# Optimization experiments

Hardware: AMD Instinct MI355X
Metric: run time of the kernel (lower is better)

## Reference

```python
import jax, jax.numpy as jnp
import numpy as np

B, C_IN, H, W = 8, 32, 64, 64
C = 64  # num_channels


def setup_inputs() -> dict:
    key = jax.random.key(0)
    ks = jax.random.split(key, 9)
    s_in = 1.0 / np.sqrt(C_IN)
    s_c = 1.0 / np.sqrt(C)
    return {
        "x": jax.random.normal(ks[0], (B, C_IN, H, W), dtype=jnp.float32),
        "wq": jax.random.uniform(ks[1], (C, C_IN), jnp.float32, -s_in, s_in),
        "bq": jax.random.uniform(ks[2], (C,), jnp.float32, -s_in, s_in),
        "wk": jax.random.uniform(ks[3], (C, C_IN), jnp.float32, -s_in, s_in),
        "bk": jax.random.uniform(ks[4], (C,), jnp.float32, -s_in, s_in),
        "wv": jax.random.uniform(ks[5], (C, C_IN), jnp.float32, -s_in, s_in),
        "bv": jax.random.uniform(ks[6], (C,), jnp.float32, -s_in, s_in),
        "wo": jax.random.uniform(ks[7], (C_IN, C), jnp.float32, -s_c, s_c),
        "bo": jax.random.uniform(ks[8], (C_IN,), jnp.float32, -s_c, s_c),
    }


def reference(x, wq, bq, wk, bk, wv, bv, wo, bo):
    b, c_in, h, w = x.shape
    n = h * w
    # 1x1 convs == per-pixel linear projections; produce (B, N, C) directly
    q = (jnp.einsum('bchw,oc->bhwo', x, wq) + bq).reshape(b, n, -1)
    k = (jnp.einsum('bchw,oc->bhwo', x, wk) + bk).reshape(b, n, -1)
    v = (jnp.einsum('bchw,oc->bhwo', x, wv) + bv).reshape(b, n, -1)
    # unscaled attention over spatial positions (no 1/sqrt(d) in original)
    scores = jnp.einsum('bnc,bmc->bnm', q, k)  # (B, N, N)
    attn = jax.nn.softmax(scores, axis=-1)
    out = jnp.einsum('bnm,bmc->bnc', attn, v)  # (B, N, C)
    out = out.reshape(b, h, w, -1)
    out = jnp.einsum('bhwc,oc->bohw', out, wo) + bo[None, :, None, None]
    return out + x
```

## Files before the change

kernel.cpp:

```cpp
#include <hip/hip_runtime.h>
#include <hip/hip_bf16.h>

#define CIN    32
#define NPIX   4096
#define DIM    64
#define LOG2E  1.4426950408889634f

#if __has_builtin(__builtin_amdgcn_exp2f)
#define EXP2(x) __builtin_amdgcn_exp2f(x)
#else
#define EXP2(x) exp2f(x)
#endif

typedef float  f32x4 __attribute__((ext_vector_type(4)));
typedef short  s16x8 __attribute__((ext_vector_type(8)));
typedef short  s16x4 __attribute__((ext_vector_type(4)));

__device__ __forceinline__ f32x4 mfma16(s16x4 a, s16x4 b, f32x4 c) {
#if __has_builtin(__builtin_amdgcn_mfma_f32_16x16x16bf16_1k)
    return __builtin_amdgcn_mfma_f32_16x16x16bf16_1k(a, b, c, 0, 0, 0);
#elif __has_builtin(__builtin_amdgcn_mfma_f32_16x16x16_bf16)
    return __builtin_amdgcn_mfma_f32_16x16x16_bf16(a, b, c, 0, 0, 0);
#else
    f32x4 d;
    asm("v_mfma_f32_16x16x16_bf16 %0, %1, %2, %3" : "=v"(d) : "v"(a), "v"(b), "v"(c));
    return d;
#endif
}


__global__ __launch_bounds__(256) void qkv_proj(
    const float* __restrict__ x,
    const float* __restrict__ wq, const float* __restrict__ bq,
    const float* __restrict__ wk, const float* __restrict__ bk,
    const float* __restrict__ wv, const float* __restrict__ bv,
    __hip_bfloat16* __restrict__ qb, __hip_bfloat16* __restrict__ kb,
    __hip_bfloat16* __restrict__ vb)
{
    __shared__ float Xs[CIN][64];
    __shared__ float wT[3][CIN][DIM];

    const int tid = threadIdx.x;
    const int b   = blockIdx.y;
    const int bx  = blockIdx.x;
    const int n0  = bx * 64;

    for (int i = tid; i < 3 * CIN * DIM; i += 256) {
        int m = i >> 11, r = i & 2047, c = r >> 6, o = r & 63;
        const float* wsrc = (m == 0) ? wq : (m == 1) ? wk : wv;
        float wv0 = wsrc[o * CIN + c];
        wT[m][c][o] = (m == 0) ? wv0 * LOG2E : wv0;
    }
    for (int i = tid * 4; i < CIN * 64; i += 1024) {
        int c = i >> 6, p = i & 63;
        *(f32x4*)&Xs[c][p] = *(const f32x4*)&x[((size_t)b * CIN + c) * NPIX + n0 + p];
    }
    __syncthreads();

    const int w    = tid >> 6;
    const int lane = tid & 63;
    const int l16  = lane >> 2;
    const int quad = lane & 3;

    const int T  = bx * 4 + w;
    const int px = T * 16 + l16;

    float aq[2][8], ak[2][8];
    #pragma unroll
    for (int kb2 = 0; kb2 < 2; kb2++) {
        f32x4 bq0 = *(const f32x4*)&bq[kb2 * 32 + quad * 8];
        f32x4 bq1 = *(const f32x4*)&bq[kb2 * 32 + quad * 8 + 4];
        f32x4 bk0 = *(const f32x4*)&bk[kb2 * 32 + quad * 8];
        f32x4 bk1 = *(const f32x4*)&bk[kb2 * 32 + quad * 8 + 4];
        #pragma unroll
        for (int j = 0; j < 4; j++) {
            aq[kb2][j] = bq0[j] * LOG2E; aq[kb2][j + 4] = bq1[j] * LOG2E;
            ak[kb2][j] = bk0[j];         ak[kb2][j + 4] = bk1[j];
        }
    }
    #pragma unroll 8
    for (int c = 0; c < CIN; c++) {
        const float xc = Xs[c][w * 16 + l16];
        #pragma unroll
        for (int kb2 = 0; kb2 < 2; kb2++) {
            f32x4 q0 = *(const f32x4*)&wT[0][c][kb2 * 32 + quad * 8];
            f32x4 q1 = *(const f32x4*)&wT[0][c][kb2 * 32 + quad * 8 + 4];
            f32x4 k0 = *(const f32x4*)&wT[1][c][kb2 * 32 + quad * 8];
            f32x4 k1 = *(const f32x4*)&wT[1][c][kb2 * 32 + quad * 8 + 4];
            #pragma unroll
            for (int j = 0; j < 4; j++) {
                aq[kb2][j]     += xc * q0[j];
                aq[kb2][j + 4] += xc * q1[j];
                ak[kb2][j]     += xc * k0[j];
                ak[kb2][j + 4] += xc * k1[j];
            }
        }
    }
    #pragma unroll
    for (int kb2 = 0; kb2 < 2; kb2++) {
        union { s16x8 v; __hip_bfloat16 h[8]; } pq, pk;
        #pragma unroll
        for (int j = 0; j < 8; j++) {
            pq.h[j] = __float2bfloat16(aq[kb2][j]);
            pk.h[j] = __float2bfloat16(ak[kb2][j]);
        }
        *(s16x8*)(qb + ((size_t)b * NPIX + px) * DIM + kb2 * 32 + quad * 8) = pq.v;
        const size_t koff =
            ((((size_t)(b * 256 + T) * 2 + kb2) * 16 + l16) * 4 + quad) * 8;
        *(s16x8*)(kb + koff) = pk.v;
    }

    const int ch = w * 16 + l16;
    float av[2][8];
    {
        const float bvc = bv[ch];
        #pragma unroll
        for (int kh = 0; kh < 2; kh++)
            #pragma unroll
            for (int j = 0; j < 8; j++) av[kh][j] = bvc;
    }
    #pragma unroll 8
    for (int c = 0; c < CIN; c++) {
        const float wvc = wT[2][c][ch];
        f32x4 x0 = *(const f32x4*)&Xs[c][quad * 8];
        f32x4 x1 = *(const f32x4*)&Xs[c][quad * 8 + 4];
        f32x4 x2 = *(const f32x4*)&Xs[c][32 + quad * 8];
        f32x4 x3 = *(const f32x4*)&Xs[c][32 + quad * 8 + 4];
        #pragma unroll
        for (int j = 0; j < 4; j++) {
            av[0][j]     += x0[j] * wvc;
            av[0][j + 4] += x1[j] * wvc;
            av[1][j]     += x2[j] * wvc;
            av[1][j + 4] += x3[j] * wvc;
        }
    }
    #pragma unroll
    for (int kh = 0; kh < 2; kh++) {
        #pragma unroll
        for (int h = 0; h < 2; h++) {
            union { unsigned long long u; __hip_bfloat16 hh[4]; } pv;
            #pragma unroll
            for (int j = 0; j < 4; j++) pv.hh[j] = __float2bfloat16(av[kh][h * 4 + j]);
            const int lanep = ((quad & 1) * 2 + h) * 16 + l16;
            const size_t chunk =
                (((size_t)(b * 128 + bx * 2 + kh) * 4 + w) * 64 + lanep) * 2 + (quad >> 1);
            *(unsigned long long*)(vb + chunk * 4) = pv.u;
        }
    }
}

__global__ __launch_bounds__(256, 4) void attn_fused(
    const __hip_bfloat16* __restrict__ qb,
    const __hip_bfloat16* __restrict__ kbf,
    const __hip_bfloat16* __restrict__ vbf,
    const float* __restrict__ wo, const float* __restrict__ bo,
    const float* __restrict__ x, float* __restrict__ y)
{
    __shared__ __align__(16) float RED[4][2][64][18];
    __shared__ float LRED[4][2][16];

    const int tid  = threadIdx.x;
    const int kq   = tid >> 6;
    const int lane = tid & 63;
    const int quad = lane >> 4, l16 = lane & 15;
    const int b    = blockIdx.x;
    const int row0 = blockIdx.y * 32;

    s16x8 qf[2][2];
    #pragma unroll
    for (int mt = 0; mt < 2; mt++)
        #pragma unroll
        for (int kb2 = 0; kb2 < 2; kb2++)
            qf[mt][kb2] = *(const s16x8*)(qb
                + ((size_t)b * NPIX + row0 + mt * 16 + l16) * DIM + kb2 * 32 + quad * 8);

    const f32x4 zero4 = {0.f, 0.f, 0.f, 0.f};
    f32x4 o[2][4];
    #pragma unroll
    for (int mt = 0; mt < 2; mt++)
        #pragma unroll
        for (int ct = 0; ct < 4; ct++) o[mt][ct] = zero4;
    f32x4 ol[2] = {zero4, zero4};

    s16x4 ones;
    #pragma unroll
    for (int j = 0; j < 4; j++) ones[j] = (short)0x3F80;

    const char* kp = (const char*)kbf + (size_t)b * 524288 + kq * 131072
                     + (l16 * 4 + quad) * 16;
    const char* vp = (const char*)vbf + (size_t)b * 524288 + kq * 131072
                     + lane * 16;

    s16x8 ck[4], cv[4];
    #pragma unroll
    for (int i = 0; i < 4; i++) {
        ck[i] = *(const s16x8*)(kp + i * 1024);
        cv[i] = *(const s16x8*)(vp + i * 1024);
    }

    for (int t = 0; t < 32; ++t) {
        kp += 4096; vp += 4096;
        f32x4 st[2][2];
        #pragma unroll
        for (int nt = 0; nt < 2; nt++)
            #pragma unroll
            for (int mt = 0; mt < 2; mt++) {
                st[nt][mt] = __builtin_amdgcn_mfma_f32_16x16x32_bf16(
                    ck[nt * 2 + 0], qf[mt][0], zero4, 0, 0, 0);
                st[nt][mt] = __builtin_amdgcn_mfma_f32_16x16x32_bf16(
                    ck[nt * 2 + 1], qf[mt][1], st[nt][mt], 0, 0, 0);
            }
        #pragma unroll
        for (int i = 0; i < 4; i++) ck[i] = *(const s16x8*)(kp + i * 1024);

        s16x4 pb[2][2];
        #pragma unroll
        for (int nt = 0; nt < 2; nt++)
            #pragma unroll
            for (int mt = 0; mt < 2; mt++) {
                f32x4 p = st[nt][mt];
                #pragma unroll
                for (int r = 0; r < 4; r++) p[r] = EXP2(p[r]);
                union { unsigned int d[2]; s16x4 v; } pk;
                pk.d[0] = (__float_as_uint(p[1]) & 0xffff0000u)
                        | (__float_as_uint(p[0]) >> 16);
                pk.d[1] = (__float_as_uint(p[3]) & 0xffff0000u)
                        | (__float_as_uint(p[2]) >> 16);
                pb[nt][mt] = pk.v;
            }

        #pragma unroll
        for (int ct = 0; ct < 4; ct++) {
            s16x4 vlo = __builtin_shufflevector(cv[ct], cv[ct], 0, 1, 2, 3);
            s16x4 vhi = __builtin_shufflevector(cv[ct], cv[ct], 4, 5, 6, 7);
            #pragma unroll
            for (int mt = 0; mt < 2; mt++) {
                o[mt][ct] = mfma16(vlo, pb[0][mt], o[mt][ct]);
                o[mt][ct] = mfma16(vhi, pb[1][mt], o[mt][ct]);
            }
        }
        #pragma unroll
        for (int mt = 0; mt < 2; mt++) {
            ol[mt] = mfma16(ones, pb[0][mt], ol[mt]);
            ol[mt] = mfma16(ones, pb[1][mt], ol[mt]);
        }
        #pragma unroll
        for (int i = 0; i < 4; i++) cv[i] = *(const s16x8*)(vp + i * 1024);
    }

    #pragma unroll
    for (int mt = 0; mt < 2; mt++) {
        #pragma unroll
        for (int ct = 0; ct < 4; ct++)
            #pragma unroll
            for (int r = 0; r < 4; r++)
                RED[kq][mt][ct * 16 + quad * 4 + r][l16] = o[mt][ct][r];
        if (quad == 0) LRED[kq][mt][l16] = ol[mt][0];
    }
    __syncthreads();

    const int emt = kq >> 1, ent = kq & 1;
    float osum[4][4];
    float lsum = 0.f;
    #pragma unroll
    for (int ct = 0; ct < 4; ct++)
        #pragma unroll
        for (int r = 0; r < 4; r++) osum[ct][r] = 0.f;
    #pragma unroll
    for (int k2 = 0; k2 < 4; k2++) {
        lsum += LRED[k2][emt][l16];
        #pragma unroll
        for (int ct = 0; ct < 4; ct++)
            #pragma unroll
            for (int r = 0; r < 4; r++)
                osum[ct][r] += RED[k2][emt][ct * 16 + quad * 4 + r][l16];
    }

    const float inv = 1.0f / lsum;
    s16x4 pvo[4];
    #pragma unroll
    for (int ct = 0; ct < 4; ct++) {
        union { s16x4 v; __hip_bfloat16 h[4]; } pk;
        #pragma unroll
        for (int r = 0; r < 4; r++)
            pk.h[r] = __float2bfloat16(osum[ct][r] * inv);
        pvo[ct] = pk.v;
    }

    s16x4 aw[4];
    #pragma unroll
    for (int ct = 0; ct < 4; ct++) {
        f32x4 w4 = *(const f32x4*)(wo + (size_t)(ent * 16 + l16) * DIM
                                   + ct * 16 + quad * 4);
        union { s16x4 v; __hip_bfloat16 h[4]; } wf;
        #pragma unroll
        for (int j = 0; j < 4; j++) wf.h[j] = __float2bfloat16(w4[j]);
        aw[ct] = wf.v;
    }

    f32x4 d2 = zero4;
    #pragma unroll
    for (int ct = 0; ct < 4; ct++)
        d2 = mfma16(aw[ct], pvo[ct], d2);

    #pragma unroll
    for (int r = 0; r < 4; r++) {
        const int out = ent * 16 + quad * 4 + r;
        const int row = row0 + emt * 16 + l16;
        const size_t xi = ((size_t)b * CIN + out) * NPIX + row;
        y[xi] = d2[r] + bo[out] + x[xi];
    }
}

extern "C" void kernel_launch(void* const* d_in, const int* in_sizes, int n_in,
                              void* d_out, int out_size, void* d_ws, size_t ws_size,
                              hipStream_t stream)
{
    const float* x  = (const float*)d_in[0];
    const float* wq = (const float*)d_in[1];
    const float* bq = (const float*)d_in[2];
    const float* wk = (const float*)d_in[3];
    const float* bk = (const float*)d_in[4];
    const float* wv = (const float*)d_in[5];
    const float* bv = (const float*)d_in[6];
    const float* wo = (const float*)d_in[7];
    const float* bo = (const float*)d_in[8];
    float* y = (float*)d_out;

    char* ws = (char*)d_ws;
    __hip_bfloat16* qb = (__hip_bfloat16*)(ws);
    __hip_bfloat16* kb = (__hip_bfloat16*)(ws + (4u << 20));
    __hip_bfloat16* vb = (__hip_bfloat16*)(ws + (8u << 20));

    qkv_proj<<<dim3(64, 8), dim3(256), 0, stream>>>(x, wq, bq, wk, bk, wv, bv, qb, kb, vb);
    attn_fused<<<dim3(8, 128), dim3(256), 0, stream>>>(qb, kb, vb, wo, bo, x, y);
}
```

Before: 137.7 us.

## Switch attention kernel to 32x32x16 MFMA tiles with re-laid-out K/V

Replaces the 16x16 MFMA tiling of the fused attention kernel with 32x32x16 bf16 MFMAs. The K and V bf16 buffers written by the projection kernel get new layouts to match. The row sum is now accumulated with scalar adds and a cross-lane shuffle instead of an MFMA against a ones vector. The cross-wave reduction is restructured so wave 0 sums the partials and alone runs the output projection and residual add. The aim is fewer MFMA issues and less shared-memory traffic per tile, at the cost of more accumulator registers and occupancy lowered from 4 to 3 blocks per CU.

```diff
diff --git a/kernel.cpp b/kernel.cpp
--- a/kernel.cpp
+++ b/kernel.cpp
@@ -12,20 +12,14 @@
 #define EXP2(x) exp2f(x)
 #endif
 
-typedef float  f32x4 __attribute__((ext_vector_type(4)));
-typedef short  s16x8 __attribute__((ext_vector_type(8)));
-typedef short  s16x4 __attribute__((ext_vector_type(4)));
-
-__device__ __forceinline__ f32x4 mfma16(s16x4 a, s16x4 b, f32x4 c) {
-#if __has_builtin(__builtin_amdgcn_mfma_f32_16x16x16bf16_1k)
-    return __builtin_amdgcn_mfma_f32_16x16x16bf16_1k(a, b, c, 0, 0, 0);
-#elif __has_builtin(__builtin_amdgcn_mfma_f32_16x16x16_bf16)
-    return __builtin_amdgcn_mfma_f32_16x16x16_bf16(a, b, c, 0, 0, 0);
-#else
-    f32x4 d;
-    asm("v_mfma_f32_16x16x16_bf16 %0, %1, %2, %3" : "=v"(d) : "v"(a), "v"(b), "v"(c));
-    return d;
-#endif
+typedef float  f32x4  __attribute__((ext_vector_type(4)));
+typedef float  f32x16 __attribute__((ext_vector_type(16)));
+typedef short  s16x8  __attribute__((ext_vector_type(8)));
+
+#define ZERO16 {0.f,0.f,0.f,0.f,0.f,0.f,0.f,0.f,0.f,0.f,0.f,0.f,0.f,0.f,0.f,0.f}
+
+__device__ __forceinline__ f32x16 mfma32(s16x8 a, s16x8 b, f32x16 c) {
+    return __builtin_amdgcn_mfma_f32_32x32x16_bf16(a, b, c, 0, 0, 0);
 }
 
 
@@ -96,18 +90,24 @@
             }
         }
     }
-    #pragma unroll
-    for (int kb2 = 0; kb2 < 2; kb2++) {
-        union { s16x8 v; __hip_bfloat16 h[8]; } pq, pk;
-        #pragma unroll
-        for (int j = 0; j < 8; j++) {
-            pq.h[j] = __float2bfloat16(aq[kb2][j]);
-            pk.h[j] = __float2bfloat16(ak[kb2][j]);
-        }
-        *(s16x8*)(qb + ((size_t)b * NPIX + px) * DIM + kb2 * 32 + quad * 8) = pq.v;
-        const size_t koff =
-            ((((size_t)(b * 256 + T) * 2 + kb2) * 16 + l16) * 4 + quad) * 8;
-        *(s16x8*)(kb + koff) = pk.v;
+    {
+        const int s   = px >> 5;
+        const int key = px & 31;
+        #pragma unroll
+        for (int kb2 = 0; kb2 < 2; kb2++) {
+            union { s16x8 v; __hip_bfloat16 h[8]; } pq, pk;
+            #pragma unroll
+            for (int j = 0; j < 8; j++) {
+                pq.h[j] = __float2bfloat16(aq[kb2][j]);
+                pk.h[j] = __float2bfloat16(ak[kb2][j]);
+            }
+            *(s16x8*)(qb + ((size_t)b * NPIX + px) * DIM + kb2 * 32 + quad * 8) = pq.v;
+            const int kt = kb2 * 2 + (quad >> 1);
+            const int h  = quad & 1;
+            const size_t koff = (size_t)b * 262144
+                + ((size_t)(s * 4 + kt) * 64 + h * 32 + key) * 8;
+            *(s16x8*)(kb + koff) = pk.v;
+        }
     }
 
     const int ch = w * 16 + l16;
@@ -136,179 +136,161 @@
     }
     #pragma unroll
     for (int kh = 0; kh < 2; kh++) {
+        const int s = bx * 2 + kh;
         #pragma unroll
         for (int h = 0; h < 2; h++) {
             union { unsigned long long u; __hip_bfloat16 hh[4]; } pv;
             #pragma unroll
             for (int j = 0; j < 4; j++) pv.hh[j] = __float2bfloat16(av[kh][h * 4 + j]);
-            const int lanep = ((quad & 1) * 2 + h) * 16 + l16;
-            const size_t chunk =
-                (((size_t)(b * 128 + bx * 2 + kh) * 4 + w) * 64 + lanep) * 2 + (quad >> 1);
-            *(unsigned long long*)(vb + chunk * 4) = pv.u;
+            const size_t voff = (size_t)b * 262144
+                + ((((size_t)(s * 2 + (ch >> 5)) * 2 + h) * 32 + (ch & 31)) * 2
+                   + (quad >> 1)) * 8
+                + 4 * (quad & 1);
+            *(unsigned long long*)(vb + voff) = pv.u;
         }
     }
 }
 
-__global__ __launch_bounds__(256, 4) void attn_fused(
+__global__ __launch_bounds__(256, 3) void attn_fused(
     const __hip_bfloat16* __restrict__ qb,
     const __hip_bfloat16* __restrict__ kbf,
     const __hip_bfloat16* __restrict__ vbf,
     const float* __restrict__ wo, const float* __restrict__ bo,
     const float* __restrict__ x, float* __restrict__ y)
 {
-    __shared__ __align__(16) float RED[4][2][64][18];
-    __shared__ float LRED[4][2][16];
+    __shared__ __align__(16) float RED[3][64][33];
+    __shared__ float LRED[3][32];
 
     const int tid  = threadIdx.x;
     const int kq   = tid >> 6;
     const int lane = tid & 63;
-    const int quad = lane >> 4, l16 = lane & 15;
+    const int q    = lane & 31;
+    const int hl   = lane >> 5;
     const int b    = blockIdx.x;
     const int row0 = blockIdx.y * 32;
 
-    s16x8 qf[2][2];
+    s16x8 qf[4];
     #pragma unroll
-    for (int mt = 0; mt < 2; mt++)
-        #pragma unroll
-        for (int kb2 = 0; kb2 < 2; kb2++)
-            qf[mt][kb2] = *(const s16x8*)(qb
-                + ((size_t)b * NPIX + row0 + mt * 16 + l16) * DIM + kb2 * 32 + quad * 8);
-
-    const f32x4 zero4 = {0.f, 0.f, 0.f, 0.f};
-    f32x4 o[2][4];
+    for (int kt = 0; kt < 4; kt++)
+        qf[kt] = *(const s16x8*)(qb + ((size_t)b * NPIX + row0 + q) * DIM
+                                 + kt * 16 + hl * 8);
+
+    f32x16 o0 = ZERO16, o1 = ZERO16;
+    float lsacc = 0.f;
+
+    const char* kp = (const char*)kbf + (size_t)b * 524288 + kq * 131072
+                     + (size_t)lane * 16;
+    const char* vp = (const char*)vbf + (size_t)b * 524288 + kq * 131072
+                     + (size_t)lane * 32;
+
+    s16x8 kA[4], kB[4], cv[4];
     #pragma unroll
-    for (int mt = 0; mt < 2; mt++)
-        #pragma unroll
-        for (int ct = 0; ct < 4; ct++) o[mt][ct] = zero4;
-    f32x4 ol[2] = {zero4, zero4};
-
-    s16x4 ones;
-    #pragma unroll
-    for (int j = 0; j < 4; j++) ones[j] = (short)0x3F80;
-
-    const char* kp = (const char*)kbf + (size_t)b * 524288 + kq * 131072
-                     + (l16 * 4 + quad) * 16;
-    const char* vp = (const char*)vbf + (size_t)b * 524288 + kq * 131072
-                     + lane * 16;
-
-    s16x8 ck[4], cv[4];
-    #pragma unroll
-    for (int i = 0; i < 4; i++) {
-        ck[i] = *(const s16x8*)(kp + i * 1024);
-        cv[i] = *(const s16x8*)(vp + i * 1024);
-    }
-
-    for (int t = 0; t < 32; ++t) {
-        kp += 4096; vp += 4096;
-        f32x4 st[2][2];
-        #pragma unroll
-        for (int nt = 0; nt < 2; nt++)
-            #pragma unroll
-            for (int mt = 0; mt < 2; mt++) {
-                st[nt][mt] = __builtin_amdgcn_mfma_f32_16x16x32_bf16(
-                    ck[nt * 2 + 0], qf[mt][0], zero4, 0, 0, 0);
-                st[nt][mt] = __builtin_amdgcn_mfma_f32_16x16x32_bf16(
-                    ck[nt * 2 + 1], qf[mt][1], st[nt][mt], 0, 0, 0);
-            }
-        #pragma unroll
-        for (int i = 0; i < 4; i++) ck[i] = *(const s16x8*)(kp + i * 1024);
-
-        s16x4 pb[2][2];
-        #pragma unroll
-        for (int nt = 0; nt < 2; nt++)
-            #pragma unroll
-            for (int mt = 0; mt < 2; mt++) {
-                f32x4 p = st[nt][mt];
-                #pragma unroll
-                for (int r = 0; r < 4; r++) p[r] = EXP2(p[r]);
-                union { unsigned int d[2]; s16x4 v; } pk;
-                pk.d[0] = (__float_as_uint(p[1]) & 0xffff0000u)
-                        | (__float_as_uint(p[0]) >> 16);
-                pk.d[1] = (__float_as_uint(p[3]) & 0xffff0000u)
-                        | (__float_as_uint(p[2]) >> 16);
-                pb[nt][mt] = pk.v;
-            }
-
-        #pragma unroll
-        for (int ct = 0; ct < 4; ct++) {
-            s16x4 vlo = __builtin_shufflevector(cv[ct], cv[ct], 0, 1, 2, 3);
-            s16x4 vhi = __builtin_shufflevector(cv[ct], cv[ct], 4, 5, 6, 7);
-            #pragma unroll
-            for (int mt = 0; mt < 2; mt++) {
-                o[mt][ct] = mfma16(vlo, pb[0][mt], o[mt][ct]);
-                o[mt][ct] = mfma16(vhi, pb[1][mt], o[mt][ct]);
-            }
-        }
-        #pragma unroll
-        for (int mt = 0; mt < 2; mt++) {
-            ol[mt] = mfma16(ones, pb[0][mt], ol[mt]);
-            ol[mt] = mfma16(ones, pb[1][mt], ol[mt]);
-        }
-        #pragma unroll
-        for (int i = 0; i < 4; i++) cv[i] = *(const s16x8*)(vp + i * 1024);
-    }
-
-    #pragma unroll
-    for (int mt = 0; mt < 2; mt++) {
-        #pragma unroll
-        for (int ct = 0; ct < 4; ct++)
-            #pragma unroll
-            for (int r = 0; r < 4; r++)
-                RED[kq][mt][ct * 16 + quad * 4 + r][l16] = o[mt][ct][r];
-        if (quad == 0) LRED[kq][mt][l16] = ol[mt][0];
+    for (int i = 0; i < 4; i++) kA[i] = *(const s16x8*)(kp + i * 1024);
+    cv[0] = *(const s16x8*)(vp + 0);
+    cv[1] = *(const s16x8*)(vp + 16);
+    cv[2] = *(const s16x8*)(vp + 2048);
+    cv[3] = *(const s16x8*)(vp + 2064);
+
+    auto step = [&](s16x8 (&cK)[4], s16x8 (&nK)[4]) {
+        kp += 4096;
+        f32x16 st = ZERO16;
+        #pragma unroll
+        for (int kt = 0; kt < 4; kt++)
+            st = mfma32(cK[kt], qf[kt], st);
+        #pragma unroll
+        for (int i = 0; i < 4; i++) nK[i] = *(const s16x8*)(kp + i * 1024);
+
+        #pragma unroll
+        for (int r = 0; r < 16; r++) { st[r] = EXP2(st[r]); lsacc += st[r]; }
+
+        union { s16x8 v; __hip_bfloat16 h8[8]; } p0, p1;
+        #pragma unroll
+        for (int j = 0; j < 8; j++) {
+            p0.h8[j] = __float2bfloat16(st[j]);
+            p1.h8[j] = __float2bfloat16(st[8 + j]);
+        }
+        o0 = mfma32(cv[0], p0.v, o0);
+        o0 = mfma32(cv[1], p1.v, o0);
+        o1 = mfma32(cv[2], p0.v, o1);
+        o1 = mfma32(cv[3], p1.v, o1);
+
+        vp += 4096;
+        cv[0] = *(const s16x8*)(vp + 0);
+        cv[1] = *(const s16x8*)(vp + 16);
+        cv[2] = *(const s16x8*)(vp + 2048);
+        cv[3] = *(const s16x8*)(vp + 2064);
+    };
+
+    for (int it = 0; it < 16; it++) {
+        step(kA, kB);
+        step(kB, kA);
+    }
+
+    lsacc += __shfl_xor(lsacc, 32, 64);
+
+    if (kq != 0) {
+        const int sl = kq - 1;
+        #pragma unroll
+        for (int i = 0; i < 16; i++) {
+            const int rr = (i & 3) + 8 * (i >> 2) + 4 * hl;
+            RED[sl][rr][q]      = o0[i];
+            RED[sl][32 + rr][q] = o1[i];
+        }
+        if (hl == 0) LRED[sl][q] = lsacc;
     }
     __syncthreads();
 
-    const int emt = kq >> 1, ent = kq & 1;
-    float osum[4][4];
-    float lsum = 0.f;
-    #pragma unroll
-    for (int ct = 0; ct < 4; ct++)
-        #pragma unroll
-        for (int r = 0; r < 4; r++) osum[ct][r] = 0.f;
-    #pragma unroll
-    for (int k2 = 0; k2 < 4; k2++) {
-        lsum += LRED[k2][emt][l16];
-        #pragma unroll
-        for (int ct = 0; ct < 4; ct++)
-            #pragma unroll
-            for (int r = 0; r < 4; r++)
-                osum[ct][r] += RED[k2][emt][ct * 16 + quad * 4 + r][l16];
-    }
-
-    const float inv = 1.0f / lsum;
-    s16x4 pvo[4];
-    #pragma unroll
-    for (int ct = 0; ct < 4; ct++) {
-        union { s16x4 v; __hip_bfloat16 h[4]; } pk;
-        #pragma unroll
-        for (int r = 0; r < 4; r++)
-            pk.h[r] = __float2bfloat16(osum[ct][r] * inv);
-        pvo[ct] = pk.v;
-    }
-
-    s16x4 aw[4];
-    #pragma unroll
-    for (int ct = 0; ct < 4; ct++) {
-        f32x4 w4 = *(const f32x4*)(wo + (size_t)(ent * 16 + l16) * DIM
-                                   + ct * 16 + quad * 4);
-        union { s16x4 v; __hip_bfloat16 h[4]; } wf;
-        #pragma unroll
-        for (int j = 0; j < 4; j++) wf.h[j] = __float2bfloat16(w4[j]);
-        aw[ct] = wf.v;
-    }
-
-    f32x4 d2 = zero4;
-    #pragma unroll
-    for (int ct = 0; ct < 4; ct++)
-        d2 = mfma16(aw[ct], pvo[ct], d2);
-
-    #pragma unroll
-    for (int r = 0; r < 4; r++) {
-        const int out = ent * 16 + quad * 4 + r;
-        const int row = row0 + emt * 16 + l16;
-        const size_t xi = ((size_t)b * CIN + out) * NPIX + row;
-        y[xi] = d2[r] + bo[out] + x[xi];
+    if (kq == 0) {
+        #pragma unroll
+        for (int sl = 0; sl < 3; sl++) {
+            lsacc += LRED[sl][q];
+            #pragma unroll
+            for (int i = 0; i < 16; i++) {
+                const int rr = (i & 3) + 8 * (i >> 2) + 4 * hl;
+                o0[i] += RED[sl][rr][q];
+                o1[i] += RED[sl][32 + rr][q];
+            }
+        }
+        const float inv = 1.0f / lsacc;
+
+        s16x8 pbo[4];
+        #pragma unroll
+        for (int g = 0; g < 4; g++) {
+            union { s16x8 v; __hip_bfloat16 h8[8]; } pk;
+            #pragma unroll
+            for (int j = 0; j < 8; j++) {
+                const float vv = (g < 2) ? o0[(g & 1) * 8 + j] : o1[(g & 1) * 8 + j];
+                pk.h8[j] = __float2bfloat16(vv * inv);
+            }
+            pbo[g] = pk.v;
+        }
+
+        s16x8 aw[4];
+        #pragma unroll
+        for (int g = 0; g < 4; g++) {
+            f32x4 w0 = *(const f32x4*)(wo + (size_t)q * DIM + g * 16 + hl * 4);
+            f32x4 w1 = *(const f32x4*)(wo + (size_t)q * DIM + g * 16 + 8 + hl * 4);
+            union { s16x8 v; __hip_bfloat16 h8[8]; } wf;
+            #pragma unroll
+            for (int j = 0; j < 4; j++) {
+                wf.h8[j]     = __float2bfloat16(w0[j]);
+                wf.h8[4 + j] = __float2bfloat16(w1[j]);
+            }
+            aw[g] = wf.v;
+        }
+
+        f32x16 d = ZERO16;
+        #pragma unroll
+        for (int g = 0; g < 4; g++)
+            d = mfma32(aw[g], pbo[g], d);
+
+        #pragma unroll
+        for (int i = 0; i < 16; i++) {
+            const int out = (i & 3) + 8 * (i >> 2) + 4 * hl;
+            const int row = row0 + q;
+            const size_t xi = ((size_t)b * CIN + out) * NPIX + row;
+            y[xi] = d[i] + bo[out] + x[xi];
+        }
     }
 }
 
```

Result: slower. 144.3 us (+4.8%).
